# Kernel optimization log

Measured on AMD Instinct MI355X. Metric: run time of the kernel, lower is better.

The kernel has to match this reference:

```python
import jax, jax.numpy as jnp
import numpy as np

R = 4          # corr_radius
SLOPE = 0.1    # leaky relu negative slope


def _conv(x, w, b, pad):
    y = jax.lax.conv_general_dilated(
        x, w, window_strides=(1, 1), padding=[(pad, pad), (pad, pad)],
        dimension_numbers=("NCHW", "OIHW", "NCHW"))
    return y + b[None, :, None, None]


def _correlation(x1, x2):
    # Fused windowed cost volume: cv[b, i*(2R+1)+j, h, w] = mean_c x1[b,c,h,w] * x2[b,c,h+i-R,w+j-R]
    B, C, H, W = x1.shape
    x2p = jnp.pad(x2, ((0, 0), (0, 0), (R, R), (R, R)))
    cv = jnp.stack(
        [jnp.mean(x1 * jax.lax.dynamic_slice(x2p, (0, 0, i, j), (B, C, H, W)), axis=1)
         for i in range(2 * R + 1) for j in range(2 * R + 1)], axis=1)
    return cv  # (B, (2R+1)^2, H, W)


def setup_inputs() -> dict:
    key = jax.random.key(0)
    ks = jax.random.split(key, 20)
    B, H, W = 2, 256, 256
    pyr = 24
    inp = {
        "feat0": jax.random.normal(ks[0], (B, 2 * pyr, H, W), jnp.float32),
        "feat1": jax.random.normal(ks[1], (B, 2 * pyr, H, W), jnp.float32),
        "last_feat": jax.random.normal(ks[2], (B, 64, H, W), jnp.float32),
        "last_flow": jax.random.normal(ks[3], (B, 4, H, W), jnp.float32),
    }
    in_ch = (2 * R + 1) ** 2 + 2 * (2 * pyr) + 64 + 4  # 245
    dims = [(160, in_ch, 1), (128, 160, 3), (112, 128, 3), (96, 112, 3), (64, 96, 3), (4, 64, 3)]
    for n, (co, ci, k) in enumerate(dims, 1):
        scale = 1.0 / np.sqrt(ci * k * k)
        inp[f"w{n}"] = jax.random.normal(ks[4 + 2 * n], (co, ci, k, k), jnp.float32) * scale
        inp[f"b{n}"] = jnp.zeros((co,), jnp.float32)
    return inp


def reference(feat0, feat1, last_feat, last_flow,
              w1, b1, w2, b2, w3, b3, w4, b4, w5, b5, w6, b6):
    lrelu = lambda x: jax.nn.leaky_relu(x, SLOPE)
    volume = lrelu(_correlation(feat0, feat1))
    feat = jnp.concatenate([volume, feat0, feat1, last_feat, last_flow], axis=1)
    x = lrelu(_conv(feat, w1, b1, 0))   # 1x1 conv
    x = lrelu(_conv(x, w2, b2, 1))
    x = lrelu(_conv(x, w3, b3, 1))
    x = lrelu(_conv(x, w4, b4, 1))
    x = lrelu(_conv(x, w5, b5, 1))
    flow = _conv(x, w6, b6, 1)          # final ConvBlock, act=None
    return flow, x
```

## Files before the change

### kernel.cpp

```cpp
#include <hip/hip_runtime.h>
#include <hip/hip_fp16.h>
#include <cstdint>
#include <cstddef>


using short8 = __attribute__((ext_vector_type(8))) short;
using f32x4  = __attribute__((ext_vector_type(4))) float;
typedef unsigned short u16;

__device__ __forceinline__ u16 rne_bf16(float f) {
  unsigned u = __float_as_uint(f);
  u += 0x7FFFu + ((u >> 16) & 1u);
  return (u16)(u >> 16);
}

__device__ __forceinline__ void mfma16(const short8& a, const short8& b, f32x4& c) {
  asm("v_mfma_f32_16x16x32_bf16 %0, %1, %2, %0" : "+v"(c) : "v"(a), "v"(b));
}

__device__ __forceinline__ unsigned pk_f16(float a, float b) {
  unsigned r;
  asm("v_cvt_pkrtz_f16_f32 %0, %1, %2" : "=v"(r) : "v"(a), "v"(b));
  return r;
}

__device__ __forceinline__ void dot2(float& acc, unsigned a, unsigned b) {
  asm("v_dot2_f32_f16 %0, %1, %2, %0" : "+v"(acc) : "v"(a), "v"(b));
}

__device__ __forceinline__ void gload16(const void* g, void* l) {
  __builtin_amdgcn_global_load_lds(
      (const __attribute__((address_space(1))) unsigned int*)g,
      (__attribute__((address_space(3))) unsigned int*)l, 16, 0, 0);
}

__device__ __forceinline__ uint2 quad_to_bf16(uint2 v) {
  __half2 lo = *(__half2*)&v.x, hi = *(__half2*)&v.y;
  uint2 u;
  u.x = (unsigned)rne_bf16(__half2float(lo.x)) | ((unsigned)rne_bf16(__half2float(lo.y)) << 16);
  u.y = (unsigned)rne_bf16(__half2float(hi.x)) | ((unsigned)rne_bf16(__half2float(hi.y)) << 16);
  return u;
}

__global__ __launch_bounds__(256) void prep1_kernel(const float* __restrict__ w1,
                                                    u16* __restrict__ w1p) {
  int idx = blockIdx.x * 256 + threadIdx.x;
  int co = idx >> 8, cip = idx & 255;
  float v = 0.f;
  if (co < 160 && cip < 245) {
    int ci = (cip < 164) ? (cip + 81) : (cip - 164);
    v = w1[co * 245 + ci];
  }
  w1p[idx] = rne_bf16(v);
}

template<int CO, int CIr, int BM, int APLN, int CIP>
__global__ __launch_bounds__(256) void prep3s_kernel(const float* __restrict__ w,
                                                     u16* __restrict__ wp) {
  int idx = blockIdx.x * 256 + threadIdx.x;
  int ci = idx % CIP; int rest = idx / CIP;
  int row = rest % APLN; int dyp = rest / APLN;
  int dx = row / BM, co = row % BM;
  float v = 0.f;
  if (dx < 3 && co < CO && ci < CIr)
    v = w[(co * CIr + ci) * 9 + dyp * 3 + dx];
  wp[idx] = rne_bf16(v);
}

template<int CO, int CI, int COP, int CIP>
__global__ __launch_bounds__(256) void prep3_kernel(const float* __restrict__ w,
                                                    u16* __restrict__ wp) {
  int idx = blockIdx.x * 256 + threadIdx.x;
  int ci = idx % CIP; int rest = idx / CIP;
  int co = rest % COP; int tap = rest / COP;
  float v = 0.f;
  if (co < CO && ci < CI) v = w[(co * CI + ci) * 9 + tap];
  wp[idx] = rne_bf16(v);
}

__global__ __launch_bounds__(256) void prep_bias_kernel(const float* __restrict__ b1,
    const float* __restrict__ b2, const float* __restrict__ b3,
    const float* __restrict__ b4, const float* __restrict__ b5,
    float* __restrict__ bp, u16* __restrict__ zbuf) {
  int i = blockIdx.x * 256 + threadIdx.x;
  if (i < 128) zbuf[i] = 0;
  float v = 0.f;
  if (i < 160) v = b1[i];
  else if (i < 288) v = b2[i - 160];
  else if (i < 416) { int c = i - 288; v = (c < 112) ? b3[c] : 0.f; }
  else if (i < 512) v = b4[i - 416];
  else if (i < 576) v = b5[i - 512];
  else return;
  bp[i] = v;
}

__global__ __launch_bounds__(256) void quadize_kernel(const float* __restrict__ f0,
                                                      const float* __restrict__ f1,
                                                      u16* __restrict__ f0q,
                                                      u16* __restrict__ f1q) {
  const int bid = blockIdx.x;
  const int qh = bid >> 9;
  const int b = (bid >> 8) & 1;
  const int h = bid & 255;
  const int hw = (h << 8) + threadIdx.x;
  const float* s0 = f0 + (((size_t)(b * 48 + qh * 24)) << 16) + hw;
  const float* s1 = f1 + (((size_t)(b * 48 + qh * 24)) << 16) + hw;
  u16* d0 = f0q + (((size_t)((b * 12 + qh * 6) << 16)) + hw) * 4;
  u16* d1 = f1q + (((size_t)((b * 12 + qh * 6) << 16)) + hw) * 4;
#pragma unroll
  for (int q = 0; q < 6; ++q) {
    uint2 u;
    u.x = pk_f16(s0[((size_t)(4 * q)) << 16],     s0[((size_t)(4 * q + 1)) << 16]);
    u.y = pk_f16(s0[((size_t)(4 * q + 2)) << 16], s0[((size_t)(4 * q + 3)) << 16]);
    *(uint2*)(d0 + (size_t)q * 262144) = u;
    uint2 v;
    v.x = pk_f16(s1[((size_t)(4 * q)) << 16],     s1[((size_t)(4 * q + 1)) << 16]);
    v.y = pk_f16(s1[((size_t)(4 * q + 2)) << 16], s1[((size_t)(4 * q + 3)) << 16]);
    *(uint2*)(d1 + (size_t)q * 262144) = v;
  }
}

__global__ __launch_bounds__(256) void concat68_kernel(const float* __restrict__ lf,
                                                       const float* __restrict__ lfl,
                                                       u16* __restrict__ X1) {
  __shared__ float s[16][68];
  const int t = threadIdx.x;
  const size_t px0 = (size_t)blockIdx.x * 64;
  const int b = blockIdx.x >> 10;
  const int hw0 = (blockIdx.x & 1023) * 64;

#pragma unroll 1
  for (int cc = 0; cc < 5; ++cc) {
    __syncthreads();
    {
      int px = t & 63, cg = t >> 6;
#pragma unroll
      for (int r = 0; r < 4; ++r) {
        int cl = cg * 4 + r;
        int c = cc * 16 + cl;
        int hw = hw0 + px;
        float v = 0.f;
        if (c < 64)       v = lf[(((size_t)(b * 64 + c)) << 16) + hw];
        else if (c < 68)  v = lfl[(((size_t)(b * 4 + (c - 64))) << 16) + hw];
        s[cl][px] = v;
      }
    }
    __syncthreads();
    {
      int px = t >> 2, g = t & 3;
      int cbase = cc * 16 + g * 4;
      if (cbase < 68) {
        ushort4 u;
        u.x = rne_bf16(s[g * 4 + 0][px]);
        u.y = rne_bf16(s[g * 4 + 1][px]);
        u.z = rne_bf16(s[g * 4 + 2][px]);
        u.w = rne_bf16(s[g * 4 + 3][px]);
        *(ushort4*)(X1 + (px0 + px) * 256 + 96 + cbase) = u;
      }
    }
  }
}

template<int NDY>
__device__ __forceinline__ void corr_acc(const uint2* __restrict__ wb,
                                         const unsigned* __restrict__ f0p,
                                         float* __restrict__ cv,
                                         int row, int col, int dy0) {
#pragma unroll
  for (int d = 0; d < NDY; ++d) {
    const int r = row + dy0 + d;
#pragma unroll
    for (int q = 0; q < 3; ++q) {
      const uint2* base = wb + (q * 10 + r) * 80 + (col + 4);
#pragma unroll
      for (int dx = 0; dx < 9; ++dx) {
        const uint2 v = base[dx];
        dot2(cv[d * 9 + dx], v.x, f0p[2 * q]);
        dot2(cv[d * 9 + dx], v.y, f0p[2 * q + 1]);
      }
    }
  }
}

__global__ __launch_bounds__(256, 4) void corr5_kernel(const u16* __restrict__ f0q,
                                                       const u16* __restrict__ f1q,
                                                       const u16* __restrict__ zbuf,
                                                       u16* __restrict__ X1) {
  __shared__ char wlds[2][20480];
  const int bid = blockIdx.x;
  const int swz = (bid & 7) * 128 + (bid >> 3);
  const int b = swz >> 9, rest = swz & 511;
  const int hp = rest >> 2, ct = rest & 3;
  const int h0 = hp << 1, w0 = ct << 6;
  const int tid = threadIdx.x, lane = tid & 63, wv = tid >> 6;
  const int half = wv >> 1, row = wv & 1, col = lane;
  const int pixhw = ((h0 + row) << 8) + (w0 + col);
  const size_t pix = ((size_t)b << 16) + pixhw;

  const u16* srcp[5];
  bool okf[5];
#pragma unroll
  for (int ru = 0; ru < 5; ++ru) {
    int u = ru * 256 + tid;
    int uq = u / 400;
    int rem = u - uq * 400;
    int r = rem / 40, cu = rem - r * 40;
    int hin = h0 + r - 4;
    int wpx = w0 - 8 + 2 * cu;
    bool ok = (u < 1200) && ((unsigned)hin < 256u) && ((unsigned)wpx < 256u);
    okf[ru] = ok;
    srcp[ru] = ok ? (f1q + (((size_t)((b * 12 + uq) << 16) + (hin << 8) + wpx) << 2))
                  : zbuf;
  }

  float cv[45];
#pragma unroll
  for (int t = 0; t < 45; ++t) cv[t] = 0.f;

#pragma unroll
  for (int ru = 0; ru < 5; ++ru)
    gload16(srcp[ru], &wlds[0][ru * 4096 + wv * 1024]);

#pragma unroll 1
  for (int cc = 0; cc < 4; ++cc) {
    __syncthreads();
    if (cc < 3) {
#pragma unroll
      for (int ru = 0; ru < 5; ++ru) {
        const u16* s = okf[ru] ? (srcp[ru] + (size_t)(cc + 1) * 786432) : zbuf;
        gload16(s, &wlds[(cc + 1) & 1][ru * 4096 + wv * 1024]);
      }
    }
    const uint2* wb = (const uint2*)&wlds[cc & 1][0];

    const u16* f0base = f0q + (((size_t)((b * 12 + cc * 3) << 16) + pixhw) << 2);
    uint2 q0 = *(const uint2*)(f0base);
    uint2 q1 = *(const uint2*)(f0base + 262144);
    uint2 q2 = *(const uint2*)(f0base + 524288);
    unsigned f0p[6] = {q0.x, q0.y, q1.x, q1.y, q2.x, q2.y};

    {
      u16* dst0 = X1 + pix * 256 + cc * 12;
      *(uint2*)(dst0)     = quad_to_bf16(q0);
      *(uint2*)(dst0 + 4) = quad_to_bf16(q1);
      *(uint2*)(dst0 + 8) = quad_to_bf16(q2);
    }
    {
      u16* dst1 = X1 + pix * 256 + 48 + cc * 12;
#pragma unroll
      for (int q = 0; q < 3; ++q) {
        uint2 v = wb[(q * 10 + row + 4) * 80 + (col + 8)];
        *(uint2*)(dst1 + 4 * q) = quad_to_bf16(v);
      }
    }
    if (half == 0) corr_acc<4>(wb, f0p, cv, row, col, 0);
    else           corr_acc<5>(wb, f0p, cv, row, col, 4);
  }

  u16* dst = X1 + pix * 256;
  const float sc = 1.0f / 48.0f;
  if (half == 0) {
#pragma unroll
    for (int qq = 0; qq < 9; ++qq) {
      u16 e[4];
#pragma unroll
      for (int j = 0; j < 4; ++j) {
        float v = cv[qq * 4 + j] * sc;
        v = v > 0.f ? v : 0.1f * v;
        e[j] = rne_bf16(v);
      }
      uint2 u;
      u.x = (unsigned)e[0] | ((unsigned)e[1] << 16);
      u.y = (unsigned)e[2] | ((unsigned)e[3] << 16);
      *(uint2*)(dst + 164 + qq * 4) = u;
    }
  } else {
#pragma unroll
    for (int qq = 0; qq < 14; ++qq) {
      u16 e[4];
#pragma unroll
      for (int j = 0; j < 4; ++j) {
        int t = qq * 4 + j;
        float v = 0.f;
        if (t < 45) {
          v = cv[t] * sc;
          v = v > 0.f ? v : 0.1f * v;
        }
        e[j] = rne_bf16(v);
      }
      uint2 u;
      u.x = (unsigned)e[0] | ((unsigned)e[1] << 16);
      u.y = (unsigned)e[2] | ((unsigned)e[3] << 16);
      *(uint2*)(dst + 200 + qq * 4) = u;
    }
  }
}

template<int CI, int BM, int APLN, int KS, int OSTRIDE, bool LRELU, bool OBF, int COF32>
__global__ __launch_bounds__(256, 2) void convr_kernel(const u16* __restrict__ Xin,
    const u16* __restrict__ Wp, const float* __restrict__ bias,
    const u16* __restrict__ zbuf, u16* __restrict__ Xout,
    float* __restrict__ outF) {
  constexpr int NCH = CI / 32;
  constexpr int NDX = (KS == 3) ? 3 : 1;
  constexpr int HALO = (KS == 3) ? 2 : 0;
  constexpr int AROUNDS = APLN / 64;
  constexpr int BROUNDS = (KS == 3) ? 5 : 4;
  constexpr int BPXMAX = 256 + 2 * HALO;
  constexpr int MF = BM / 32;
  constexpr int AELEMS = AROUNDS * 2048;
  constexpr int NPH = NDX * NCH;
  __shared__ u16 lds[AELEMS + BROUNDS * 2048];

  const int tid = threadIdx.x;
  const int lane = tid & 63, wv = tid >> 6;
  const int wm = wv >> 1, wn = wv & 1;
  const int bid = blockIdx.x;
  const int swz = (bid & 7) * 64 + (bid >> 3);
  const int bi = swz >> 8;
  const int h = swz & 255;
  const int l15 = lane & 15, segr = lane >> 4;

  size_t aofs[AROUNDS];
#pragma unroll
  for (int r = 0; r < AROUNDS; ++r) {
    int slot = r * 256 + tid;
    int row = slot >> 2, sp = slot & 3;
    int seg = sp ^ ((row >> 1) & 3);
    aofs[r] = (size_t)row * CI + seg * 8;
  }
  size_t bofs[BROUNDS];
  bool bcolv[BROUNDS];
#pragma unroll
  for (int r = 0; r < BROUNDS; ++r) {
    int slot = r * 256 + tid;
    int pxl = slot >> 2, sp = slot & 3;
    int seg = sp ^ ((pxl >> 1) & 3);
    int px = pxl - HALO;
    bcolv[r] = ((unsigned)px < 256u) && (pxl < BPXMAX);
    bofs[r] = (size_t)px * CI + seg * 8;
  }

  f32x4 acc[MF][8];
  const f32x4 zf = {0.f, 0.f, 0.f, 0.f};
#pragma unroll
  for (int m = 0; m < MF; ++m)
#pragma unroll
    for (int n = 0; n < 8; ++n) acc[m][n] = zf;

  const int ph0 = (((bid >> 8) ^ bid) & 1) * (NPH / 2);

#pragma unroll 1
  for (int i = 0; i < NPH; ++i) {
    int ph = ph0 + i;
    if (ph >= NPH) ph -= NPH;
    const int dy = ph / NCH;
    const int c = ph - dy * NCH;
    __syncthreads();
    const u16* Wph = Wp + ((size_t)dy * APLN) * CI + c * 32;
#pragma unroll
    for (int r = 0; r < AROUNDS; ++r)
      gload16(Wph + aofs[r], &lds[r * 2048 + wv * 512]);
    const int hin = (KS == 3) ? (h + dy - 1) : h;
    const bool rv = (unsigned)hin < 256u;
    const u16* Brow = Xin + ((size_t)((bi << 8) + (rv ? hin : 0)) << 8) * CI + c * 32;
#pragma unroll
    for (int r = 0; r < BROUNDS; ++r) {
      const u16* src = (rv && bcolv[r]) ? (Brow + bofs[r]) : zbuf;
      gload16(src, &lds[AELEMS + r * 2048 + wv * 512]);
    }
    __syncthreads();

#pragma unroll
    for (int dx = 0; dx < NDX; ++dx) {
      short8 bfr[8];
#pragma unroll
      for (int n = 0; n < 8; ++n) {
        int p = wn * 128 + n * 16 + l15;
        int pxl = (KS == 3) ? (p + dx + 1) : p;
        int ba = (AELEMS * 2) + pxl * 64 + ((segr ^ ((pxl >> 1) & 3)) << 4);
        bfr[n] = *(const short8*)((const char*)lds + ba);
      }
      short8 afr[MF];
#pragma unroll
      for (int m = 0; m < MF; ++m) {
        int row = dx * BM + wm * (BM / 2) + m * 16 + l15;
        int aa = row * 64 + ((segr ^ ((row >> 1) & 3)) << 4);
        afr[m] = *(const short8*)((const char*)lds + aa);
      }
#pragma unroll
      for (int m = 0; m < MF; ++m)
#pragma unroll
        for (int n = 0; n < 8; ++n) mfma16(afr[m], bfr[n], acc[m][n]);
    }
  }
  asm volatile("s_nop 7\n\ts_nop 7");

  const int co_sub = (lane >> 4) << 2;
  const size_t pixbase = ((size_t)((bi << 8) + h)) << 8;
#pragma unroll
  for (int m = 0; m < MF; ++m) {
    const int co = wm * (BM / 2) + m * 16 + co_sub;
#pragma unroll
    for (int n = 0; n < 8; ++n) {
      const int px = wn * 128 + n * 16 + l15;
      f32x4 v = acc[m][n];
      float t[4];
#pragma unroll
      for (int r = 0; r < 4; ++r) {
        float x = v[r] + bias[co + r];
        if (LRELU) x = x > 0.f ? x : 0.1f * x;
        t[r] = x;
      }
      if (OBF) {
        ushort4 u;
        u.x = rne_bf16(t[0]); u.y = rne_bf16(t[1]);
        u.z = rne_bf16(t[2]); u.w = rne_bf16(t[3]);
        *(ushort4*)(Xout + (pixbase + px) * OSTRIDE + co) = u;
      }
      if (COF32 > 0) {
#pragma unroll
        for (int r = 0; r < 4; ++r) {
          int cch = co + r;
          if (cch < COF32)
            outF[(((size_t)bi * COF32 + cch) << 16) + (h << 8) + px] = t[r];
        }
      }
    }
  }
}

template<int CI, int COP, int MF, int KS, bool LRELU, bool OBF, int COF32>
__global__ __launch_bounds__(256) void conv_kernel(const u16* __restrict__ Xin,
                                                   const u16* __restrict__ Wp,
                                                   const float* __restrict__ bias,
                                                   u16* __restrict__ Xout, int ostride,
                                                   float* __restrict__ outF) {
  const int lane = threadIdx.x & 63, wv = threadIdx.x >> 6;
  const int bi = blockIdx.x >> 9;
  const int h = (blockIdx.x >> 1) & 255;
  const int w0 = (blockIdx.x & 1) << 7;
  const int co0 = blockIdx.y * (MF * 16);
  const int l15 = lane & 15, klane = (lane >> 4) << 3;
  const int ncol0 = w0 + wv * 32 + l15;
  const int rowbase = (bi << 8) + h;

  const f32x4 zf = {0.f, 0.f, 0.f, 0.f};
  const short8 z8 = {0, 0, 0, 0, 0, 0, 0, 0};
  f32x4 acc[MF][2];
#pragma unroll
  for (int m = 0; m < MF; ++m) { acc[m][0] = zf; acc[m][1] = zf; }

#pragma unroll 1
  for (int chunk = 0; chunk < CI / 32; ++chunk) {
#pragma unroll
    for (int tap = 0; tap < KS * KS; ++tap) {
      const int dy = (KS == 3) ? tap / 3 - 1 : 0;
      const int dx = (KS == 3) ? tap % 3 - 1 : 0;
      const int hin = h + dy;
      if (KS == 3 && (unsigned)hin >= 256u) continue;
      short8 bf[2];
#pragma unroll
      for (int nf = 0; nf < 2; ++nf) {
        int win = ncol0 + nf * 16 + dx;
        short8 v = z8;
        if (KS == 1 || (unsigned)win < 256u)
          v = *(const short8*)(Xin + ((size_t)(((bi << 8) + hin) * 256 + win)) * CI
                               + chunk * 32 + klane);
        bf[nf] = v;
      }
#pragma unroll
      for (int m = 0; m < MF; ++m) {
        const short8 af = *(const short8*)(Wp + ((size_t)(tap * COP + co0 + m * 16 + l15)) * CI
                                           + chunk * 32 + klane);
        mfma16(af, bf[0], acc[m][0]);
        mfma16(af, bf[1], acc[m][1]);
      }
    }
  }
  asm volatile("s_nop 7\n\ts_nop 7");

  const int co_sub = (lane >> 4) << 2;
  const size_t pixrow = (size_t)rowbase << 8;
#pragma unroll
  for (int m = 0; m < MF; ++m) {
    const int co = co0 + m * 16 + co_sub;
#pragma unroll
    for (int nf = 0; nf < 2; ++nf) {
      const int w = ncol0 + nf * 16;
      f32x4 v = acc[m][nf];
      if constexpr (OBF) {
        float t[4];
#pragma unroll
        for (int r = 0; r < 4; ++r) {
          float x = v[r] + bias[co + r];
          if constexpr (LRELU) x = x > 0.f ? x : 0.1f * x;
          t[r] = x;
        }
        ushort4 u;
        u.x = rne_bf16(t[0]); u.y = rne_bf16(t[1]);
        u.z = rne_bf16(t[2]); u.w = rne_bf16(t[3]);
        *(ushort4*)(Xout + (pixrow + w) * (size_t)ostride + co) = u;
      }
      if constexpr (COF32 > 0) {
#pragma unroll
        for (int r = 0; r < 4; ++r) {
          int c = co + r;
          if (c < COF32) {
            float x = v[r] + bias[c];
            if constexpr (LRELU) x = x > 0.f ? x : 0.1f * x;
            outF[((((size_t)bi * COF32) + c) << 16) + (h << 8) + w] = x;
          }
        }
      }
    }
  }
}

extern "C" void kernel_launch(void* const* d_in, const int* in_sizes, int n_in,
                              void* d_out, int out_size, void* d_ws, size_t ws_size,
                              hipStream_t stream) {
  const float* feat0 = (const float*)d_in[0];
  const float* feat1 = (const float*)d_in[1];
  const float* lfeat = (const float*)d_in[2];
  const float* lflow = (const float*)d_in[3];
  const float* w1 = (const float*)d_in[4];  const float* b1 = (const float*)d_in[5];
  const float* w2 = (const float*)d_in[6];  const float* b2 = (const float*)d_in[7];
  const float* w3 = (const float*)d_in[8];  const float* b3 = (const float*)d_in[9];
  const float* w4 = (const float*)d_in[10]; const float* b4 = (const float*)d_in[11];
  const float* w5 = (const float*)d_in[12]; const float* b5 = (const float*)d_in[13];
  const float* w6 = (const float*)d_in[14]; const float* b6 = (const float*)d_in[15];

  u16* ws = (u16*)d_ws;
  u16* X1 = ws;
  u16* X2 = ws + 33554432;
  u16* X3 = ws;
  u16* X4 = ws + 33554432;
  u16* X5 = ws;
  u16* X6 = ws + 33554432;
  u16* f0q = ws + 33554432;
  u16* f1q = ws + 39845888;
  u16* w1p = ws + 54525952;
  u16* w2p = w1p + 49152;
  u16* w3p = w2p + 184320;
  u16* w4p = w3p + 147456;
  u16* w5p = w4p + 147456;
  u16* w6p = w5p + 55296;
  float* bp = (float*)(w6p + 9216);
  u16* zbuf = (u16*)(bp + 576);

  const float* bp1 = bp;
  const float* bp2 = bp + 160;
  const float* bp3 = bp + 288;
  const float* bp4 = bp + 416;
  const float* bp5 = bp + 512;

  float* flow = (float*)d_out;
  float* xout = (float*)d_out + 524288;

  prep1_kernel<<<192, 256, 0, stream>>>(w1, w1p);
  prep3s_kernel<128, 160, 128, 384, 160><<<720, 256, 0, stream>>>(w2, w2p);
  prep3s_kernel<112, 128, 128, 384, 128><<<576, 256, 0, stream>>>(w3, w3p);
  prep3s_kernel< 96, 112,  96, 320, 128><<<480, 256, 0, stream>>>(w4, w4p);
  prep3s_kernel< 64,  96,  64, 192,  96><<<216, 256, 0, stream>>>(w5, w5p);
  prep3_kernel<  4,  64,  16,  64><<< 36, 256, 0, stream>>>(w6, w6p);
  prep_bias_kernel<<<3, 256, 0, stream>>>(b1, b2, b3, b4, b5, bp, zbuf);

  quadize_kernel<<<1024, 256, 0, stream>>>(feat0, feat1, f0q, f1q);
  concat68_kernel<<<2048, 256, 0, stream>>>(lfeat, lflow, X1);
  corr5_kernel<<<1024, 256, 0, stream>>>(f0q, f1q, zbuf, X1);

  convr_kernel<256, 160, 192, 1, 160, true, true,  0><<<512, 256, 0, stream>>>(X1, w1p, bp1, zbuf, X2, nullptr);
  convr_kernel<160, 128, 384, 3, 128, true, true,  0><<<512, 256, 0, stream>>>(X2, w2p, bp2, zbuf, X3, nullptr);
  convr_kernel<128, 128, 384, 3, 128, true, true,  0><<<512, 256, 0, stream>>>(X3, w3p, bp3, zbuf, X4, nullptr);
  convr_kernel<128,  96, 320, 3,  96, true, true,  0><<<512, 256, 0, stream>>>(X4, w4p, bp4, zbuf, X5, nullptr);
  convr_kernel< 96,  64, 192, 3,  64, true, true, 64><<<512, 256, 0, stream>>>(X5, w5p, bp5, zbuf, X6, xout);
  conv_kernel< 64,  16, 1, 3, false, false, 4><<<dim3(1024, 1), 256, 0, stream>>>(X6, w6p, b6, nullptr, 0, flow);
}
```

Before: 299.6 us.

## Double-buffer conv LDS stages with 512-thread blocks and MFMA priority scheduling

Replaces the 256-thread single-buffered conv kernel with a 512-thread, one-block-per-CU version that double-buffers weight and input tiles in LDS. The next phase is prefetched through global_load_lds while the current one is computed, using explicit vmcnt waits instead of syncthreads. Each wave now covers 64 pixels instead of 128. MFMA issue is bracketed by barriers and setprio so waves interleave their LDS reads and math. Weight padding is enlarged to fit the new 128-row load granularity, and the per-q barriers add synchronisation overhead.

```diff
diff --git a/kernel.cpp b/kernel.cpp
--- a/kernel.cpp
+++ b/kernel.cpp
@@ -32,6 +32,14 @@
   __builtin_amdgcn_global_load_lds(
       (const __attribute__((address_space(1))) unsigned int*)g,
       (__attribute__((address_space(3))) unsigned int*)l, 16, 0, 0);
+}
+
+template<int N> __device__ __forceinline__ void wait_vm() {
+  if constexpr (N == 0)      asm volatile("s_waitcnt vmcnt(0)" ::: "memory");
+  else if constexpr (N == 4) asm volatile("s_waitcnt vmcnt(4)" ::: "memory");
+  else if constexpr (N == 5) asm volatile("s_waitcnt vmcnt(5)" ::: "memory");
+  else if constexpr (N == 6) asm volatile("s_waitcnt vmcnt(6)" ::: "memory");
+  else                       asm volatile("s_waitcnt vmcnt(0)" ::: "memory");
 }
 
 __device__ __forceinline__ uint2 quad_to_bf16(uint2 v) {
@@ -296,44 +304,45 @@
   }
 }
 
-template<int CI, int BM, int APLN, int KS, int OSTRIDE, bool LRELU, bool OBF, int COF32>
-__global__ __launch_bounds__(256, 2) void convr_kernel(const u16* __restrict__ Xin,
+template<int CI, int BM, int AR, int KS, int OSTRIDE, bool LRELU, bool OBF, int COF32>
+__global__ __launch_bounds__(512, 1) void convp_kernel(const u16* __restrict__ Xin,
     const u16* __restrict__ Wp, const float* __restrict__ bias,
     const u16* __restrict__ zbuf, u16* __restrict__ Xout,
     float* __restrict__ outF) {
   constexpr int NCH = CI / 32;
   constexpr int NDX = (KS == 3) ? 3 : 1;
   constexpr int HALO = (KS == 3) ? 2 : 0;
-  constexpr int AROUNDS = APLN / 64;
-  constexpr int BROUNDS = (KS == 3) ? 5 : 4;
+  constexpr int BR = (KS == 3) ? 3 : 2;
   constexpr int BPXMAX = 256 + 2 * HALO;
   constexpr int MF = BM / 32;
-  constexpr int AELEMS = AROUNDS * 2048;
+  constexpr int AELEMS = AR * 4096;
+  constexpr int BELEMS = BR * 4096;
   constexpr int NPH = NDX * NCH;
-  __shared__ u16 lds[AELEMS + BROUNDS * 2048];
+  constexpr int LOADS = AR + BR;
+  __shared__ u16 lds[2][AELEMS + BELEMS];
 
   const int tid = threadIdx.x;
   const int lane = tid & 63, wv = tid >> 6;
-  const int wm = wv >> 1, wn = wv & 1;
+  const int wm = wv >> 2, wn = wv & 3;
   const int bid = blockIdx.x;
   const int swz = (bid & 7) * 64 + (bid >> 3);
   const int bi = swz >> 8;
   const int h = swz & 255;
   const int l15 = lane & 15, segr = lane >> 4;
 
-  size_t aofs[AROUNDS];
-#pragma unroll
-  for (int r = 0; r < AROUNDS; ++r) {
-    int slot = r * 256 + tid;
+  size_t aofs[AR];
+#pragma unroll
+  for (int r = 0; r < AR; ++r) {
+    int slot = r * 512 + tid;
     int row = slot >> 2, sp = slot & 3;
     int seg = sp ^ ((row >> 1) & 3);
     aofs[r] = (size_t)row * CI + seg * 8;
   }
-  size_t bofs[BROUNDS];
-  bool bcolv[BROUNDS];
-#pragma unroll
-  for (int r = 0; r < BROUNDS; ++r) {
-    int slot = r * 256 + tid;
+  size_t bofs[BR];
+  bool bcolv[BR];
+#pragma unroll
+  for (int r = 0; r < BR; ++r) {
+    int slot = r * 512 + tid;
     int pxl = slot >> 2, sp = slot & 3;
     int seg = sp ^ ((pxl >> 1) & 3);
     int px = pxl - HALO;
@@ -341,57 +350,79 @@
     bofs[r] = (size_t)px * CI + seg * 8;
   }
 
-  f32x4 acc[MF][8];
-  const f32x4 zf = {0.f, 0.f, 0.f, 0.f};
-#pragma unroll
-  for (int m = 0; m < MF; ++m)
-#pragma unroll
-    for (int n = 0; n < 8; ++n) acc[m][n] = zf;
-
-  const int ph0 = (((bid >> 8) ^ bid) & 1) * (NPH / 2);
-
-#pragma unroll 1
-  for (int i = 0; i < NPH; ++i) {
-    int ph = ph0 + i;
-    if (ph >= NPH) ph -= NPH;
+  auto stage = [&](int ph, int bsel) {
     const int dy = ph / NCH;
     const int c = ph - dy * NCH;
-    __syncthreads();
-    const u16* Wph = Wp + ((size_t)dy * APLN) * CI + c * 32;
-#pragma unroll
-    for (int r = 0; r < AROUNDS; ++r)
-      gload16(Wph + aofs[r], &lds[r * 2048 + wv * 512]);
+    const u16* Wph = Wp + ((size_t)dy * (AR * 128)) * CI + c * 32;
+#pragma unroll
+    for (int r = 0; r < AR; ++r)
+      gload16(Wph + aofs[r], &lds[bsel][r * 4096 + wv * 512]);
     const int hin = (KS == 3) ? (h + dy - 1) : h;
     const bool rv = (unsigned)hin < 256u;
     const u16* Brow = Xin + ((size_t)((bi << 8) + (rv ? hin : 0)) << 8) * CI + c * 32;
 #pragma unroll
-    for (int r = 0; r < BROUNDS; ++r) {
+    for (int r = 0; r < BR; ++r) {
       const u16* src = (rv && bcolv[r]) ? (Brow + bofs[r]) : zbuf;
-      gload16(src, &lds[AELEMS + r * 2048 + wv * 512]);
-    }
-    __syncthreads();
-
-#pragma unroll
-    for (int dx = 0; dx < NDX; ++dx) {
-      short8 bfr[8];
-#pragma unroll
-      for (int n = 0; n < 8; ++n) {
-        int p = wn * 128 + n * 16 + l15;
-        int pxl = (KS == 3) ? (p + dx + 1) : p;
-        int ba = (AELEMS * 2) + pxl * 64 + ((segr ^ ((pxl >> 1) & 3)) << 4);
-        bfr[n] = *(const short8*)((const char*)lds + ba);
-      }
-      short8 afr[MF];
+      gload16(src, &lds[bsel][AELEMS + r * 4096 + wv * 512]);
+    }
+  };
+
+  f32x4 acc[MF][4];
+  const f32x4 zf = {0.f, 0.f, 0.f, 0.f};
+#pragma unroll
+  for (int m = 0; m < MF; ++m)
+#pragma unroll
+    for (int n = 0; n < 4; ++n) acc[m][n] = zf;
+
+  stage(0, 0);
+  wait_vm<0>();
+  __builtin_amdgcn_s_barrier();
+
+#pragma unroll 1
+  for (int t = 0; t < NPH; ++t) {
+    const int buf = t & 1;
+    if (t + 1 < NPH) {
+      stage(t + 1, buf ^ 1);
+      wait_vm<LOADS>();
+    } else {
+      wait_vm<0>();
+    }
+    __builtin_amdgcn_s_barrier();
+
+    const char* Abase = (const char*)&lds[buf][0];
+    const char* Bbase = (const char*)&lds[buf][AELEMS];
+
+    short8 afr[NDX * MF];
+#pragma unroll
+    for (int dx = 0; dx < NDX; ++dx)
 #pragma unroll
       for (int m = 0; m < MF; ++m) {
         int row = dx * BM + wm * (BM / 2) + m * 16 + l15;
         int aa = row * 64 + ((segr ^ ((row >> 1) & 3)) << 4);
-        afr[m] = *(const short8*)((const char*)lds + aa);
-      }
-#pragma unroll
-      for (int m = 0; m < MF; ++m)
-#pragma unroll
-        for (int n = 0; n < 8; ++n) mfma16(afr[m], bfr[n], acc[m][n]);
+        afr[dx * MF + m] = *(const short8*)(Abase + aa);
+      }
+
+#pragma unroll
+    for (int q = 0; q < 4; ++q) {
+      short8 bfr[NDX];
+#pragma unroll
+      for (int dx = 0; dx < NDX; ++dx) {
+        int p = wn * 64 + q * 16 + l15;
+        int pxl = (KS == 3) ? (p + dx + 1) : p;
+        int ba = pxl * 64 + ((segr ^ ((pxl >> 1) & 3)) << 4);
+        bfr[dx] = *(const short8*)(Bbase + ba);
+      }
+      __builtin_amdgcn_s_barrier();
+      asm volatile("s_waitcnt lgkmcnt(0)" ::: "memory");
+      __builtin_amdgcn_sched_barrier(0);
+      __builtin_amdgcn_s_setprio(1);
+#pragma unroll
+      for (int dx = 0; dx < NDX; ++dx)
+#pragma unroll
+        for (int m = 0; m < MF; ++m)
+          mfma16(afr[dx * MF + m], bfr[dx], acc[m][q]);
+      __builtin_amdgcn_s_setprio(0);
+      __builtin_amdgcn_s_barrier();
     }
   }
   asm volatile("s_nop 7\n\ts_nop 7");
@@ -402,8 +433,8 @@
   for (int m = 0; m < MF; ++m) {
     const int co = wm * (BM / 2) + m * 16 + co_sub;
 #pragma unroll
-    for (int n = 0; n < 8; ++n) {
-      const int px = wn * 128 + n * 16 + l15;
+    for (int n = 0; n < 4; ++n) {
+      const int px = wn * 64 + n * 16 + l15;
       f32x4 v = acc[m][n];
       float t[4];
 #pragma unroll
@@ -541,11 +572,11 @@
   u16* f0q = ws + 33554432;
   u16* f1q = ws + 39845888;
   u16* w1p = ws + 54525952;
-  u16* w2p = w1p + 49152;
+  u16* w2p = w1p + 65536;
   u16* w3p = w2p + 184320;
   u16* w4p = w3p + 147456;
   u16* w5p = w4p + 147456;
-  u16* w6p = w5p + 55296;
+  u16* w6p = w5p + 73728;
   float* bp = (float*)(w6p + 9216);
   u16* zbuf = (u16*)(bp + 576);
 
@@ -558,11 +589,11 @@
   float* flow = (float*)d_out;
   float* xout = (float*)d_out + 524288;
 
-  prep1_kernel<<<192, 256, 0, stream>>>(w1, w1p);
+  prep1_kernel<<<256, 256, 0, stream>>>(w1, w1p);
   prep3s_kernel<128, 160, 128, 384, 160><<<720, 256, 0, stream>>>(w2, w2p);
   prep3s_kernel<112, 128, 128, 384, 128><<<576, 256, 0, stream>>>(w3, w3p);
-  prep3s_kernel< 96, 112,  96, 320, 128><<<480, 256, 0, stream>>>(w4, w4p);
-  prep3s_kernel< 64,  96,  64, 192,  96><<<216, 256, 0, stream>>>(w5, w5p);
+  prep3s_kernel< 96, 112,  96, 384, 128><<<576, 256, 0, stream>>>(w4, w4p);
+  prep3s_kernel< 64,  96,  64, 256,  96><<<288, 256, 0, stream>>>(w5, w5p);
   prep3_kernel<  4,  64,  16,  64><<< 36, 256, 0, stream>>>(w6, w6p);
   prep_bias_kernel<<<3, 256, 0, stream>>>(b1, b2, b3, b4, b5, bp, zbuf);
 
@@ -570,10 +601,10 @@
   concat68_kernel<<<2048, 256, 0, stream>>>(lfeat, lflow, X1);
   corr5_kernel<<<1024, 256, 0, stream>>>(f0q, f1q, zbuf, X1);
 
-  convr_kernel<256, 160, 192, 1, 160, true, true,  0><<<512, 256, 0, stream>>>(X1, w1p, bp1, zbuf, X2, nullptr);
-  convr_kernel<160, 128, 384, 3, 128, true, true,  0><<<512, 256, 0, stream>>>(X2, w2p, bp2, zbuf, X3, nullptr);
-  convr_kernel<128, 128, 384, 3, 128, true, true,  0><<<512, 256, 0, stream>>>(X3, w3p, bp3, zbuf, X4, nullptr);
-  convr_kernel<128,  96, 320, 3,  96, true, true,  0><<<512, 256, 0, stream>>>(X4, w4p, bp4, zbuf, X5, nullptr);
-  convr_kernel< 96,  64, 192, 3,  64, true, true, 64><<<512, 256, 0, stream>>>(X5, w5p, bp5, zbuf, X6, xout);
+  convp_kernel<256, 160, 2, 1, 160, true, true,  0><<<512, 512, 0, stream>>>(X1, w1p, bp1, zbuf, X2, nullptr);
+  convp_kernel<160, 128, 3, 3, 128, true, true,  0><<<512, 512, 0, stream>>>(X2, w2p, bp2, zbuf, X3, nullptr);
+  convp_kernel<128, 128, 3, 3, 128, true, true,  0><<<512, 512, 0, stream>>>(X3, w3p, bp3, zbuf, X4, nullptr);
+  convp_kernel<128,  96, 3, 3,  96, true, true,  0><<<512, 512, 0, stream>>>(X4, w4p, bp4, zbuf, X5, nullptr);
+  convp_kernel< 96,  64, 2, 3,  64, true, true, 64><<<512, 512, 0, stream>>>(X5, w5p, bp5, zbuf, X6, xout);
   conv_kernel< 64,  16, 1, 3, false, false, 4><<<dim3(1024, 1), 256, 0, stream>>>(X6, w6p, b6, nullptr, 0, flow);
 }
```

After: 333.1 us. +11.2%, slower.
